# Kernel tuning notes

Hardware: AMD Instinct MI355X
Metric: run time of the kernel (lower is better)

The kernel has to match this reference:

```python
import jax, jax.numpy as jnp
import numpy as np

SEQ_LEN = 200
BATCH = 4096
V = 50000


def setup_inputs() -> dict:
    key = jax.random.key(0)
    k1, k2, k3 = jax.random.split(key, 3)
    text = jax.random.randint(k1, (SEQ_LEN, BATCH), 0, V, dtype=jnp.int64)
    W = jax.random.normal(k2, (1, V), dtype=jnp.float32)
    b = jax.random.normal(k3, (1,), dtype=jnp.float32)
    return {"text": text, "W": W, "b": b}


def reference(text, W, b):
    # text: [L, B] int token ids. Original builds word_vecs[phrase, val] += 1
    # iterating over Counter KEYS -> binary presence indicator per document.
    L, B = text.shape
    rows = jnp.arange(B)[:, None]                      # [B, 1]
    word_vecs = jnp.zeros((B, V), dtype=jnp.float32).at[rows, text.T].set(1.0)  # [B, V]
    # nn.Linear(V, 1): y = x @ W.T + b
    return word_vecs @ W.T + b                          # [B, 1]
```

## Files before the change

kernel.cpp:

```cpp
#include <hip/hip_runtime.h>

constexpr int SEQ_LEN = 200;
constexpr int BATCH   = 4096;
constexpr int V       = 50000;
constexpr int V_WORDS = (V + 31) / 32;

__global__ __launch_bounds__(256) void MNB_8151847928093_kernel(
    const int*   __restrict__ text,
    const float* __restrict__ W,
    const float* __restrict__ bias,
    float*       __restrict__ out)
{
    __shared__ unsigned int bitmap[V_WORDS];
    __shared__ float partial[4];

    const int b   = blockIdx.x;
    const int tid = threadIdx.x;

    for (int i = tid; i < V_WORDS; i += 256) bitmap[i] = 0u;
    __syncthreads();

    float sum = 0.0f;
    if (tid < SEQ_LEN) {
        const int tok = text[tid * BATCH + b];
        const unsigned int m   = 1u << (tok & 31);
        const unsigned int old = atomicOr(&bitmap[tok >> 5], m);
        if (!(old & m)) sum = W[tok];
    }

    #pragma unroll
    for (int off = 32; off > 0; off >>= 1)
        sum += __shfl_down(sum, off, 64);

    const int wave = tid >> 6;
    const int lane = tid & 63;
    if (lane == 0) partial[wave] = sum;
    __syncthreads();

    if (tid == 0)
        out[b] = partial[0] + partial[1] + partial[2] + partial[3] + bias[0];
}

extern "C" void kernel_launch(void* const* d_in, const int* in_sizes, int n_in,
                              void* d_out, int out_size, void* d_ws, size_t ws_size,
                              hipStream_t stream) {
    const int*   text = (const int*)d_in[0];
    const float* W    = (const float*)d_in[1];
    const float* bias = (const float*)d_in[2];
    float*       out  = (float*)d_out;

    MNB_8151847928093_kernel<<<BATCH, 256, 0, stream>>>(text, W, bias, out);
}
```

Before: 64.91 us.

## Replace per-document shared bitmap with per-doc hash tables, 16 docs per block

Replaces the 6.25KB-per-document shared-memory bitmap, which had to be zeroed for every document, with a small open-addressing hash table per document (512 slots) using atomicCAS for dedup. Each 512-thread block now handles 16 documents, with the doc index in the low thread bits so text loads coalesce across adjacent batch columns. This is meant to remove the dominant bitmap-clearing cost and the poorly coalesced single-column loads. In exchange it adds hashing, possible probe loops, and a 32KB hash table per block.

```diff
diff --git a/kernel.cpp b/kernel.cpp
--- a/kernel.cpp
+++ b/kernel.cpp
@@ -3,42 +3,61 @@
 constexpr int SEQ_LEN = 200;
 constexpr int BATCH   = 4096;
 constexpr int V       = 50000;
-constexpr int V_WORDS = (V + 31) / 32;
 
-__global__ __launch_bounds__(256) void MNB_8151847928093_kernel(
+constexpr int DOCS    = 16;
+constexpr int NTHR    = 512;
+constexpr int SLICES  = NTHR / DOCS;
+constexpr int TOK_PT  = (SEQ_LEN + SLICES - 1) / SLICES;
+constexpr int HSLOTS  = 512;
+constexpr unsigned EMPTY = 0xFFFFFFFFu;
+
+__global__ __launch_bounds__(NTHR) void MNB_8151847928093_kernel(
     const int*   __restrict__ text,
     const float* __restrict__ W,
     const float* __restrict__ bias,
     float*       __restrict__ out)
 {
-    __shared__ unsigned int bitmap[V_WORDS];
-    __shared__ float partial[4];
+    __shared__ unsigned ht[HSLOTS * DOCS];
+    __shared__ float    psum[SLICES * DOCS];
 
-    const int b   = blockIdx.x;
-    const int tid = threadIdx.x;
+    const int tid   = threadIdx.x;
+    const int doc   = tid & (DOCS - 1);
+    const int slice = tid >> 4;
+    const int b     = blockIdx.x * DOCS + doc;
 
-    for (int i = tid; i < V_WORDS; i += 256) bitmap[i] = 0u;
+    for (int i = tid; i < HSLOTS * DOCS; i += NTHR) ht[i] = EMPTY;
     __syncthreads();
 
-    float sum = 0.0f;
-    if (tid < SEQ_LEN) {
-        const int tok = text[tid * BATCH + b];
-        const unsigned int m   = 1u << (tok & 31);
-        const unsigned int old = atomicOr(&bitmap[tok >> 5], m);
-        if (!(old & m)) sum = W[tok];
+    unsigned toks[TOK_PT];
+    #pragma unroll
+    for (int i = 0; i < TOK_PT; ++i) {
+        const int t = slice + i * SLICES;
+        toks[i] = (t < SEQ_LEN) ? (unsigned)text[t * BATCH + b] : EMPTY;
     }
 
+    float sum = 0.0f;
     #pragma unroll
-    for (int off = 32; off > 0; off >>= 1)
-        sum += __shfl_down(sum, off, 64);
+    for (int i = 0; i < TOK_PT; ++i) {
+        const unsigned tok = toks[i];
+        if (tok == EMPTY) continue;
+        unsigned slot = ((tok * 2654435761u) >> 16) & (HSLOTS - 1);
+        while (true) {
+            const unsigned old = atomicCAS(&ht[slot * DOCS + doc], EMPTY, tok);
+            if (old == EMPTY) { sum += W[tok]; break; }
+            if (old == tok)   { break; }
+            slot = (slot + 1) & (HSLOTS - 1);
+        }
+    }
 
-    const int wave = tid >> 6;
-    const int lane = tid & 63;
-    if (lane == 0) partial[wave] = sum;
+    psum[slice * DOCS + doc] = sum;
     __syncthreads();
 
-    if (tid == 0)
-        out[b] = partial[0] + partial[1] + partial[2] + partial[3] + bias[0];
+    if (tid < DOCS) {
+        float s = bias[0];
+        #pragma unroll
+        for (int k = 0; k < SLICES; ++k) s += psum[k * DOCS + tid];
+        out[blockIdx.x * DOCS + tid] = s;
+    }
 }
 
 extern "C" void kernel_launch(void* const* d_in, const int* in_sizes, int n_in,
@@ -49,5 +68,5 @@
     const float* bias = (const float*)d_in[2];
     float*       out  = (float*)d_out;
 
-    MNB_8151847928093_kernel<<<BATCH, 256, 0, stream>>>(text, W, bias, out);
+    MNB_8151847928093_kernel<<<BATCH / DOCS, NTHR, 0, stream>>>(text, W, bias, out);
 }
```

Measured after the change: 65.88 us. No clear change (+1.5%).
